# Kernel tuning notes

Measured on AMD Instinct MI355X. Metric: run time of the kernel, lower is better.

The kernel has to match this reference:

```python
import jax, jax.numpy as jnp
import numpy as np

BLOCK = 32      # MX block size (elements sharing one scale)
EMAX = 8        # e4m3 max biased-unbias exponent (max normal = 448 = 2^8 * 1.75)
EMIN = -6       # e4m3 min normal exponent (values below handled as subnormal grid)
MAN_BITS = 3    # e4m3 mantissa bits
MAXVAL = 448.0  # e4m3 max representable magnitude


def _fp8_e4m3(x):
    """Round x to the nearest FP8 E4M3 representable value (saturating)."""
    absx = jnp.abs(x)
    # exponent of each element, clipped to normal range; EMIN clip gives the subnormal grid
    e = jnp.clip(jnp.floor(jnp.log2(jnp.where(absx > 0, absx, 1.0))), EMIN, EMAX)
    quantum = jnp.exp2(e - MAN_BITS)          # spacing of representable values at this exponent
    q = jnp.round(absx / quantum) * quantum   # round-to-nearest on that grid
    return jnp.sign(x) * jnp.minimum(q, MAXVAL)


def mx_fake_quant(x):
    """MX (microscaling) fake quantization: per-32-element power-of-two shared
    scale from block amax, elements stored as FP8 E4M3, then dequantized."""
    shape = x.shape
    xb = x.reshape(-1, BLOCK)                                   # [n_blocks, 32]
    amax = jnp.max(jnp.abs(xb), axis=-1, keepdims=True)         # [n_blocks, 1]
    # shared exponent: floor(log2(amax)) - emax_elem  (E8M0 power-of-two scale)
    shared_exp = jnp.floor(jnp.log2(jnp.where(amax > 0, amax, 1.0))) - EMAX
    scale = jnp.exp2(shared_exp)
    xq = _fp8_e4m3(xb / scale) * scale
    return xq.reshape(shape)


@jax.custom_vjp
def mx_ste(x):
    return mx_fake_quant(x)


def _mx_fwd(x):
    return mx_fake_quant(x), None


def _mx_bwd(_, g):
    return (g,)  # straight-through estimator


mx_ste.defvjp(_mx_fwd, _mx_bwd)


def setup_inputs() -> dict:
    key = jax.random.key(0)
    k1, k2 = jax.random.split(key)
    d_in, d_out = 256, 256
    x = jax.random.normal(k1, (16, 8192, d_in), dtype=jnp.float32)
    # lecun_normal init: std = 1/sqrt(fan_in)
    kernel = jax.random.normal(k2, (d_in, d_out), dtype=jnp.float32) * (1.0 / np.sqrt(d_in))
    bias = jnp.zeros((d_out,), dtype=jnp.float32)
    return {"x": x, "kernel": kernel, "bias": bias}


def reference(x, kernel, bias):
    xq = mx_ste(x)        # quantize_input=True
    kq = mx_ste(kernel)   # weight quantizer
    return jnp.dot(xq, kq) + bias
```

## Files before the change

kernel.cpp:

```cpp
#include <hip/hip_runtime.h>
#include <hip/hip_bf16.h>

typedef unsigned short u16;
typedef unsigned int u32;
typedef __attribute__((ext_vector_type(8))) short bf16x8;
typedef __attribute__((ext_vector_type(4))) float f32x4;
typedef __attribute__((ext_vector_type(2))) float f32x2;
typedef __attribute__((ext_vector_type(4))) unsigned short u16x4;

#define NBLK 256

__device__ __forceinline__ void block_scale(float amax, float& scale, float& inv_scale) {
    int be = (int)(__float_as_uint(amax) >> 23);
    be = be < 8 ? 8 : be;
    scale     = __uint_as_float((unsigned)(be - 8) << 23);
    inv_scale = __uint_as_float((unsigned)(262 - be) << 23);
}

#if __has_builtin(__builtin_amdgcn_cvt_pk_fp8_f32) && __has_builtin(__builtin_amdgcn_cvt_pk_f32_fp8)
#define HAS_HW_FP8 1
#else
#define HAS_HW_FP8 0
#endif

#if !HAS_HW_FP8
__device__ __forceinline__ float mx_e4m3(float x, float inv_scale, float scale) {
    float v  = x * inv_scale;
    float av = fabsf(v);
    int e = (int)(__float_as_uint(av) >> 23) - 127;
    e = e < -6 ? -6 : (e > 8 ? 8 : e);
    float qs = __uint_as_float((unsigned)(130 - e) << 23);
    float qm = __uint_as_float((unsigned)(124 + e) << 23);
    float q  = fminf(rintf(av * qs) * qm, 448.0f);
    return copysignf(q, v) * scale;
}
#endif

__device__ __forceinline__ u16x4 quant4(float4 v, float inv, float sc) {
    u16x4 r;
#if HAS_HW_FP8
    float a = fminf(fmaxf(v.x * inv, -448.f), 448.f);
    float b = fminf(fmaxf(v.y * inv, -448.f), 448.f);
    float c = fminf(fmaxf(v.z * inv, -448.f), 448.f);
    float d = fminf(fmaxf(v.w * inv, -448.f), 448.f);
    int p = __builtin_amdgcn_cvt_pk_fp8_f32(a, b, 0, false);
    p     = __builtin_amdgcn_cvt_pk_fp8_f32(c, d, p, true);
    f32x2 lo = __builtin_amdgcn_cvt_pk_f32_fp8(p, false);
    f32x2 hi = __builtin_amdgcn_cvt_pk_f32_fp8(p, true);
    r.x = (u16)(__float_as_uint(lo[0] * sc) >> 16);
    r.y = (u16)(__float_as_uint(lo[1] * sc) >> 16);
    r.z = (u16)(__float_as_uint(hi[0] * sc) >> 16);
    r.w = (u16)(__float_as_uint(hi[1] * sc) >> 16);
#else
    r.x = (u16)(__float_as_uint(mx_e4m3(v.x, inv, sc)) >> 16);
    r.y = (u16)(__float_as_uint(mx_e4m3(v.y, inv, sc)) >> 16);
    r.z = (u16)(__float_as_uint(mx_e4m3(v.z, inv, sc)) >> 16);
    r.w = (u16)(__float_as_uint(mx_e4m3(v.w, inv, sc)) >> 16);
#endif
    return r;
}

__global__ void wq_kernel(const float* __restrict__ W, u16* __restrict__ Bq) {
    const int t  = blockIdx.x * blockDim.x + threadIdx.x;
    const int f  = t * 4;
    const int k  = f >> 8;
    const int n0 = f & 255;
    const float4 v = *(const float4*)(W + f);
    float am = fmaxf(fmaxf(fabsf(v.x), fabsf(v.y)), fmaxf(fabsf(v.z), fabsf(v.w)));
    am = fmaxf(am, __shfl_xor(am, 1));
    am = fmaxf(am, __shfl_xor(am, 2));
    am = fmaxf(am, __shfl_xor(am, 4));
    float sc, inv; block_scale(am, sc, inv);
    u16x4 q = quant4(v, inv, sc);
    Bq[(size_t)(n0 + 0) * 256 + k] = q.x;
    Bq[(size_t)(n0 + 1) * 256 + k] = q.y;
    Bq[(size_t)(n0 + 2) * 256 + k] = q.z;
    Bq[(size_t)(n0 + 3) * 256 + k] = q.w;
}

__global__ void __launch_bounds__(512, 1)
mx_gemm(const float* __restrict__ X, const u16* __restrict__ Bq,
        const float* __restrict__ bias, float* __restrict__ out)
{
    __shared__ u16   Bs[256 * 256];
    __shared__ float bs[256];
    const int tid = threadIdx.x;
    const int w   = tid >> 6;
    const int l   = tid & 63;
    const int lr  = l & 15;
    const int lg  = l >> 4;
    const size_t rowblk = (size_t)blockIdx.x * 512;

    #pragma unroll
    for (int i = 0; i < 16; ++i) {
        const u32 g   = (u32)(tid + i * 512) * 16;
        const u32 n   = g >> 9;
        const u32 kc  = (g >> 4) & 31;
        const u32 ks  = kc >> 2;
        const u32 lgd = kc & 3;
        const u32 d   = (n >> 4) * 8192 + ks * 1024
                      + ((((lgd << 4) | (n & 15)) ^ (ks * 9)) << 4);
        *(bf16x8*)((char*)Bs + d) = *(const bf16x8*)((const char*)Bq + g);
    }
    if (tid < 256) bs[tid] = bias[tid];
    __syncthreads();

    const u32   lslot = (u32)(lg * 16 + lr);
    const char* BsB   = (const char*)Bs;

    #pragma unroll 1
    for (int s = 0; s < 2; ++s) {
        const size_t rowt0 = rowblk + (size_t)s * 256 + (size_t)w * 16;

        bf16x8 af0[8], af1[8];
        #pragma unroll
        for (int half = 0; half < 2; ++half) {
            const float* xp = X + (rowt0 + (size_t)half * 128 + lr) * 256 + lg * 8;
            float4 xv[16];
            #pragma unroll
            for (int kp = 0; kp < 8; ++kp) {
                xv[2 * kp]     = *(const float4*)(xp + kp * 32);
                xv[2 * kp + 1] = *(const float4*)(xp + kp * 32 + 4);
            }
            #pragma unroll
            for (int ks = 0; ks < 8; ++ks) {
                const float4 v0 = xv[2 * ks], v1 = xv[2 * ks + 1];
                float am = fmaxf(fmaxf(fabsf(v0.x), fabsf(v0.y)), fmaxf(fabsf(v0.z), fabsf(v0.w)));
                am = fmaxf(am, fmaxf(fmaxf(fabsf(v1.x), fabsf(v1.y)), fmaxf(fabsf(v1.z), fabsf(v1.w))));
                am = fmaxf(am, __shfl_xor(am, 16));
                am = fmaxf(am, __shfl_xor(am, 32));
                float sc, inv; block_scale(am, sc, inv);
                const u16x4 q0 = quant4(v0, inv, sc);
                const u16x4 q1 = quant4(v1, inv, sc);
                bf16x8 a;
                a[0] = (short)q0.x; a[1] = (short)q0.y; a[2] = (short)q0.z; a[3] = (short)q0.w;
                a[4] = (short)q1.x; a[5] = (short)q1.y; a[6] = (short)q1.z; a[7] = (short)q1.w;
                if (half == 0) af0[ks] = a; else af1[ks] = a;
            }
        }

        float* op0 = out + (rowt0 + lr) * 256 + lg * 4;
        float* op1 = op0 + (size_t)128 * 256;
        #pragma unroll
        for (int h = 0; h < 4; ++h) {
            f32x4 acc0[4], acc1[4];
            #pragma unroll
            for (int ct = 0; ct < 4; ++ct) {
                const f32x4 bv = *(const f32x4*)(bs + (h * 4 + ct) * 16 + lg * 4);
                acc0[ct] = bv; acc1[ct] = bv;
            }
            #pragma unroll
            for (int ks = 0; ks < 8; ++ks) {
                #pragma unroll
                for (int ct = 0; ct < 4; ++ct) {
                    const u32 off = (u32)(h * 4 + ct) * 8192 + (u32)ks * 1024
                                  + ((lslot ^ (u32)(ks * 9)) << 4);
                    const bf16x8 bf = *(const bf16x8*)(BsB + off);
                    acc0[ct] = __builtin_amdgcn_mfma_f32_16x16x32_bf16(bf, af0[ks], acc0[ct], 0, 0, 0);
                    acc1[ct] = __builtin_amdgcn_mfma_f32_16x16x32_bf16(bf, af1[ks], acc1[ct], 0, 0, 0);
                }
            }
            #pragma unroll
            for (int ct = 0; ct < 4; ++ct) {
                *(f32x4*)(op0 + (h * 4 + ct) * 16) = acc0[ct];
                *(f32x4*)(op1 + (h * 4 + ct) * 16) = acc1[ct];
            }
        }

        if (s < 1) __builtin_amdgcn_s_barrier();
    }
}

extern "C" void kernel_launch(void* const* d_in, const int* in_sizes, int n_in,
                              void* d_out, int out_size, void* d_ws, size_t ws_size,
                              hipStream_t stream) {
    const float* x    = (const float*)d_in[0];
    const float* wk   = (const float*)d_in[1];
    const float* bias = (const float*)d_in[2];
    float* out = (float*)d_out;
    u16* Bq    = (u16*)d_ws;
    wq_kernel<<<64, 256, 0, stream>>>(wk, Bq);
    mx_gemm<<<NBLK, 512, 0, stream>>>(x, Bq, bias, out);
}
```

Baseline: 61.43 us.

## Prefetch next stage's X rows into registers and set waves-per-EU hint

During stage 0, the kernel issues the global loads for the first half of stage 1's X rows into a register buffer, so those loads overlap the current quantization and MFMA work. sched_barrier calls pin the load ordering. The launch bounds change from (512,1) to waves_per_eu(2,2), which alters the register budget the compiler may use. The extra 16 float4 registers per thread raise register pressure and could cause spills or lower occupancy.

```diff
diff --git a/kernel.cpp b/kernel.cpp
--- a/kernel.cpp
+++ b/kernel.cpp
@@ -78,7 +78,8 @@
     Bq[(size_t)(n0 + 3) * 256 + k] = q.w;
 }
 
-__global__ void __launch_bounds__(512, 1)
+__global__ void __launch_bounds__(512)
+__attribute__((amdgpu_waves_per_eu(2, 2)))
 mx_gemm(const float* __restrict__ X, const u16* __restrict__ Bq,
         const float* __restrict__ bias, float* __restrict__ out)
 {
@@ -108,14 +109,16 @@
     const u32   lslot = (u32)(lg * 16 + lr);
     const char* BsB   = (const char*)Bs;
 
+    float4 xvN[16];
+
     #pragma unroll 1
     for (int s = 0; s < 2; ++s) {
         const size_t rowt0 = rowblk + (size_t)s * 256 + (size_t)w * 16;
 
         bf16x8 af0[8], af1[8];
-        #pragma unroll
-        for (int half = 0; half < 2; ++half) {
-            const float* xp = X + (rowt0 + (size_t)half * 128 + lr) * 256 + lg * 8;
+
+        if (s == 0) {
+            const float* xp = X + (rowt0 + lr) * 256 + lg * 8;
             float4 xv[16];
             #pragma unroll
             for (int kp = 0; kp < 8; ++kp) {
@@ -135,9 +138,60 @@
                 bf16x8 a;
                 a[0] = (short)q0.x; a[1] = (short)q0.y; a[2] = (short)q0.z; a[3] = (short)q0.w;
                 a[4] = (short)q1.x; a[5] = (short)q1.y; a[6] = (short)q1.z; a[7] = (short)q1.w;
-                if (half == 0) af0[ks] = a; else af1[ks] = a;
+                af0[ks] = a;
+            }
+        } else {
+            #pragma unroll
+            for (int ks = 0; ks < 8; ++ks) {
+                const float4 v0 = xvN[2 * ks], v1 = xvN[2 * ks + 1];
+                float am = fmaxf(fmaxf(fabsf(v0.x), fabsf(v0.y)), fmaxf(fabsf(v0.z), fabsf(v0.w)));
+                am = fmaxf(am, fmaxf(fmaxf(fabsf(v1.x), fabsf(v1.y)), fmaxf(fabsf(v1.z), fabsf(v1.w))));
+                am = fmaxf(am, __shfl_xor(am, 16));
+                am = fmaxf(am, __shfl_xor(am, 32));
+                float sc, inv; block_scale(am, sc, inv);
+                const u16x4 q0 = quant4(v0, inv, sc);
+                const u16x4 q1 = quant4(v1, inv, sc);
+                bf16x8 a;
+                a[0] = (short)q0.x; a[1] = (short)q0.y; a[2] = (short)q0.z; a[3] = (short)q0.w;
+                a[4] = (short)q1.x; a[5] = (short)q1.y; a[6] = (short)q1.z; a[7] = (short)q1.w;
+                af0[ks] = a;
             }
         }
+
+        {
+            const float* xp = X + (rowt0 + 128 + lr) * 256 + lg * 8;
+            float4 xv[16];
+            #pragma unroll
+            for (int kp = 0; kp < 8; ++kp) {
+                xv[2 * kp]     = *(const float4*)(xp + kp * 32);
+                xv[2 * kp + 1] = *(const float4*)(xp + kp * 32 + 4);
+            }
+            if (s == 0) {
+                const float* xn = X + (rowblk + 256 + (size_t)w * 16 + lr) * 256 + lg * 8;
+                #pragma unroll
+                for (int kp = 0; kp < 8; ++kp) {
+                    xvN[2 * kp]     = *(const float4*)(xn + kp * 32);
+                    xvN[2 * kp + 1] = *(const float4*)(xn + kp * 32 + 4);
+                }
+            }
+            __builtin_amdgcn_sched_barrier(0);
+            #pragma unroll
+            for (int ks = 0; ks < 8; ++ks) {
+                const float4 v0 = xv[2 * ks], v1 = xv[2 * ks + 1];
+                float am = fmaxf(fmaxf(fabsf(v0.x), fabsf(v0.y)), fmaxf(fabsf(v0.z), fabsf(v0.w)));
+                am = fmaxf(am, fmaxf(fmaxf(fabsf(v1.x), fabsf(v1.y)), fmaxf(fabsf(v1.z), fabsf(v1.w))));
+                am = fmaxf(am, __shfl_xor(am, 16));
+                am = fmaxf(am, __shfl_xor(am, 32));
+                float sc, inv; block_scale(am, sc, inv);
+                const u16x4 q0 = quant4(v0, inv, sc);
+                const u16x4 q1 = quant4(v1, inv, sc);
+                bf16x8 a;
+                a[0] = (short)q0.x; a[1] = (short)q0.y; a[2] = (short)q0.z; a[3] = (short)q0.w;
+                a[4] = (short)q1.x; a[5] = (short)q1.y; a[6] = (short)q1.z; a[7] = (short)q1.w;
+                af1[ks] = a;
+            }
+        }
+        __builtin_amdgcn_sched_barrier(0);
 
         float* op0 = out + (rowt0 + lr) * 256 + lg * 4;
         float* op1 = op0 + (size_t)128 * 256;
```

New measurement: 58.39 us (median of 2 runs). 4.9% less time.
